# Kernel optimization log

Hardware: AMD Instinct MI355X
Metric: run time of the kernel (lower is better)

## Reference

```python
import jax, jax.numpy as jnp
import numpy as np

L, C = 32768, 512
EPS = 1e-5

def _layernorm(x, w, b):
    mu = jnp.mean(x, axis=-1, keepdims=True)
    var = jnp.mean(jnp.square(x - mu), axis=-1, keepdims=True)
    return (x - mu) * jax.lax.rsqrt(var + EPS) * w + b

def _scan(u, decay):
    # inclusive first-order linear scan: b_t = decay * b_{t-1} + u_t
    a = jnp.broadcast_to(decay, u.shape)
    def combine(l, r):
        return (l[0] * r[0], r[1] + r[0] * l[1])
    _, b = jax.lax.associative_scan(combine, (a, u), axis=0)
    return b

def setup_inputs() -> dict:
    key = jax.random.key(0)
    ks = jax.random.split(key, 8)
    s = 0.02
    return {
        "x": jax.random.normal(ks[0], (L, C), dtype=jnp.float32),
        "ln1_w": jnp.ones((C,), jnp.float32),
        "ln1_b": jnp.zeros((C,), jnp.float32),
        "W_in": jax.random.normal(ks[1], (C, C), jnp.float32) * s,
        "b_in": jnp.zeros((C,), jnp.float32),
        "W_gate": jax.random.normal(ks[2], (C, C), jnp.float32) * s,
        "b_gate": jnp.zeros((C,), jnp.float32),
        "W_out": jax.random.normal(ks[3], (C, C), jnp.float32) * s,
        "b_out": jnp.zeros((C,), jnp.float32),
        "decay_logit": jnp.zeros((C,), jnp.float32),  # torch init: zeros -> sigmoid = 0.5
        "ln2_w": jnp.ones((C,), jnp.float32),
        "ln2_b": jnp.zeros((C,), jnp.float32),
        "W_ff1": jax.random.normal(ks[4], (C, 2 * C), jnp.float32) * s,
        "b_ff1": jnp.zeros((2 * C,), jnp.float32),
        "W_ff2": jax.random.normal(ks[5], (2 * C, C), jnp.float32) * s,
        "b_ff2": jnp.zeros((C,), jnp.float32),
    }

def reference(x, ln1_w, ln1_b, W_in, b_in, W_gate, b_gate, W_out, b_out,
              decay_logit, ln2_w, ln2_b, W_ff1, b_ff1, W_ff2, b_ff2):
    hidden = _layernorm(x, ln1_w, ln1_b)
    u = hidden @ W_in + b_in
    gate = jax.nn.sigmoid(hidden @ W_gate + b_gate)
    decay = jax.nn.sigmoid(decay_logit)
    fwd = _scan(u, decay) * gate
    bwd = jnp.flip(_scan(jnp.flip(u, axis=0), decay), axis=0) * gate
    state_out = 0.5 * (fwd + bwd)
    x = x + state_out @ W_out + b_out
    h = _layernorm(x, ln2_w, ln2_b)
    x = x + jax.nn.silu(h @ W_ff1 + b_ff1) @ W_ff2 + b_ff2
    return x
```

## Files before the change

### kernel.cpp

```cpp
#include <hip/hip_runtime.h>
#include <stdint.h>


#define L_SEQ 32768
#define CDIM 512
#define LN_EPS 1e-5f
#define CHUNK 64
#define NCHUNK (L_SEQ / CHUNK)

typedef __attribute__((ext_vector_type(8))) short short8;
typedef __attribute__((ext_vector_type(4))) float floatx4;

__device__ inline unsigned short f2bf(float f) {
  union { float f; unsigned int u; } v; v.f = f;
  unsigned int r = v.u + 0x7fffu + ((v.u >> 16) & 1u);
  return (unsigned short)(r >> 16);
}
__device__ inline float bf2f(unsigned short h) {
  union { float f; unsigned int u; } v; v.u = ((unsigned int)h) << 16;
  return v.f;
}
__device__ inline float sigmoidf_(float x) { return 1.0f / (1.0f + __expf(-x)); }

__device__ inline void async16(const void* g, void* l) {
  __builtin_amdgcn_global_load_lds(
      (const __attribute__((address_space(1))) unsigned int*)g,
      (__attribute__((address_space(3))) unsigned int*)l, 16, 0, 0);
}

__global__ __launch_bounds__(256) void ln_kernel(const float* __restrict__ x,
    const float* __restrict__ w, const float* __restrict__ b,
    unsigned short* __restrict__ out) {
  int row = blockIdx.x * 4 + (threadIdx.x >> 6);
  int lane = threadIdx.x & 63;
  const float4* xr = (const float4*)(x + (size_t)row * CDIM);
  float4 v0 = xr[lane * 2];
  float4 v1 = xr[lane * 2 + 1];
  float s = v0.x + v0.y + v0.z + v0.w + v1.x + v1.y + v1.z + v1.w;
  float s2 = v0.x * v0.x + v0.y * v0.y + v0.z * v0.z + v0.w * v0.w +
             v1.x * v1.x + v1.y * v1.y + v1.z * v1.z + v1.w * v1.w;
  for (int m = 32; m > 0; m >>= 1) {
    s += __shfl_xor(s, m, 64);
    s2 += __shfl_xor(s2, m, 64);
  }
  float mean = s * (1.0f / CDIM);
  float var = s2 * (1.0f / CDIM) - mean * mean;
  float rs = rsqrtf(var + LN_EPS);
  const float4* wr = (const float4*)w;
  const float4* br = (const float4*)b;
  float4 w0 = wr[lane * 2], w1 = wr[lane * 2 + 1];
  float4 b0 = br[lane * 2], b1 = br[lane * 2 + 1];
  unsigned int p0 = (unsigned int)f2bf((v0.x - mean) * rs * w0.x + b0.x) |
                    ((unsigned int)f2bf((v0.y - mean) * rs * w0.y + b0.y) << 16);
  unsigned int p1 = (unsigned int)f2bf((v0.z - mean) * rs * w0.z + b0.z) |
                    ((unsigned int)f2bf((v0.w - mean) * rs * w0.w + b0.w) << 16);
  unsigned int p2 = (unsigned int)f2bf((v1.x - mean) * rs * w1.x + b1.x) |
                    ((unsigned int)f2bf((v1.y - mean) * rs * w1.y + b1.y) << 16);
  unsigned int p3 = (unsigned int)f2bf((v1.z - mean) * rs * w1.z + b1.z) |
                    ((unsigned int)f2bf((v1.w - mean) * rs * w1.w + b1.w) << 16);
  uint4 pk; pk.x = p0; pk.y = p1; pk.z = p2; pk.w = p3;
  *((uint4*)(out + (size_t)row * CDIM + lane * 8)) = pk;
}

__global__ __launch_bounds__(256) void transpose_w(const float* __restrict__ W,
    unsigned short* __restrict__ Wt, int K, int N) {
  __shared__ float tile[32][33];
  int n0 = blockIdx.x * 32, k0 = blockIdx.y * 32;
  int tx = threadIdx.x & 31, ty = threadIdx.x >> 5;
  for (int r = 0; r < 32; r += 8)
    tile[ty + r][tx] = W[(size_t)(k0 + ty + r) * N + n0 + tx];
  __syncthreads();
  for (int r = 0; r < 32; r += 8)
    Wt[(size_t)(n0 + ty + r) * K + k0 + tx] = f2bf(tile[tx][ty + r]);
}

__global__ void decay_prep(const float* __restrict__ logit,
    float* __restrict__ decay, float* __restrict__ decayT) {
  int c = threadIdx.x;
  float d = sigmoidf_(logit[c]);
  decay[c] = d;
  float p = d;
  for (int i = 0; i < 6; i++) p *= p;
  decayT[c] = p;
}

template <int EPI>
__global__ __launch_bounds__(256, 3) void gemm_bt(
    const unsigned short* __restrict__ A, const unsigned short* __restrict__ Bt,
    const float* __restrict__ biasA, const float* __restrict__ biasB,
    const float* __restrict__ res, float* __restrict__ outF,
    unsigned short* __restrict__ outU, unsigned short* __restrict__ outG,
    int M, int N, int K) {
  __shared__ unsigned short As[2][128 * 32];
  __shared__ unsigned short Bs[2][128 * 32];

  int nbx = gridDim.x, nby = gridDim.y;
  int bid = blockIdx.x + blockIdx.y * nbx;
  int per = (nbx * nby) >> 3;
  int w = (bid & 7) * per + (bid >> 3);
  int ni = w % nby;
  int mi = w / nby;
  int bm = mi << 7, bn = ni << 7;

  int tid = threadIdx.x, wave = tid >> 6, lane = tid & 63;
  int wm = (wave >> 1) * 64, wn = (wave & 1) * 64;

  int srow = wave * 16 + (lane >> 2);
  int scol = (lane & 3) * 8;
  const unsigned short* aP0 = A + (size_t)(bm + srow) * K + scol;
  const unsigned short* aP1 = A + (size_t)(bm + 64 + srow) * K + scol;
  const unsigned short* bP0 = Bt + (size_t)(bn + srow) * K + scol;
  const unsigned short* bP1 = Bt + (size_t)(bn + 64 + srow) * K + scol;

  floatx4 acc[4][4];
#pragma unroll
  for (int i = 0; i < 4; i++)
#pragma unroll
    for (int j = 0; j < 4; j++) acc[i][j] = (floatx4){0.f, 0.f, 0.f, 0.f};

  int quad = lane >> 4, r16 = lane & 15;

  async16(aP0, &As[0][wave * 512]);
  async16(aP1, &As[0][2048 + wave * 512]);
  async16(bP0, &Bs[0][wave * 512]);
  async16(bP1, &Bs[0][2048 + wave * 512]);

  for (int k0 = 0; k0 < K; k0 += 32) {
    int cur = (k0 >> 5) & 1, nxt = cur ^ 1;
    __syncthreads();
    if (k0 + 32 < K) {
      async16(aP0 + k0 + 32, &As[nxt][wave * 512]);
      async16(aP1 + k0 + 32, &As[nxt][2048 + wave * 512]);
      async16(bP0 + k0 + 32, &Bs[nxt][wave * 512]);
      async16(bP1 + k0 + 32, &Bs[nxt][2048 + wave * 512]);
    }
    short8 af[4], bfm[4];
#pragma unroll
    for (int i = 0; i < 4; i++)
      af[i] = *(const short8*)(&As[cur][(wm + i * 16 + r16) * 32 + quad * 8]);
#pragma unroll
    for (int j = 0; j < 4; j++)
      bfm[j] = *(const short8*)(&Bs[cur][(wn + j * 16 + r16) * 32 + quad * 8]);
#pragma unroll
    for (int i = 0; i < 4; i++)
#pragma unroll
      for (int j = 0; j < 4; j++)
        acc[i][j] = __builtin_amdgcn_mfma_f32_16x16x32_bf16(af[i], bfm[j], acc[i][j], 0, 0, 0);
  }

#pragma unroll
  for (int j = 0; j < 4; j++) {
    int n = bn + wn + j * 16 + r16;
#pragma unroll
    for (int i = 0; i < 4; i++) {
      int mb = bm + wm + i * 16 + quad * 4;
#pragma unroll
      for (int r = 0; r < 4; r++) {
        int m = mb + r;
        float v = acc[i][j][r];
        if (EPI == 0) {
          if (n < 512) {
            outU[(size_t)m * 512 + n] = f2bf(v + biasA[n]);
          } else {
            outG[(size_t)m * 512 + (n - 512)] = f2bf(sigmoidf_(v + biasB[n - 512]));
          }
        } else if (EPI == 1) {
          size_t idx = (size_t)m * N + n;
          outF[idx] = res[idx] + v + biasA[n];
        } else {
          float t = v + biasA[n];
          outG[(size_t)m * N + n] = f2bf(t * sigmoidf_(t));
        }
      }
    }
  }
}

__global__ __launch_bounds__(512) void scan_phase1(const unsigned short* __restrict__ u,
    const float* __restrict__ decay, float* __restrict__ fa, float* __restrict__ ba) {
  int c = threadIdx.x, k = blockIdx.x;
  float d = decay[c];
  const unsigned short* up = u + (size_t)k * CHUNK * CDIM + c;
  float f = 0.f, bs = 0.f, p = 1.f;
#pragma unroll 8
  for (int t = 0; t < CHUNK; t++) {
    float v = bf2f(up[(size_t)t * CDIM]);
    f = d * f + v;
    bs += p * v;
    p *= d;
  }
  fa[(size_t)k * CDIM + c] = f;
  ba[(size_t)k * CDIM + c] = bs;
}

__global__ __launch_bounds__(256) void scan_phase2(const float* __restrict__ fa,
    const float* __restrict__ ba, const float* __restrict__ decayT,
    float* __restrict__ fc, float* __restrict__ bc) {
  int c = blockIdx.x * 256 + threadIdx.x;
  float dT = decayT[c];
  float run = 0.f;
#pragma unroll 8
  for (int k = 0; k < NCHUNK; k++) {
    fc[(size_t)k * CDIM + c] = run;
    run = dT * run + fa[(size_t)k * CDIM + c];
  }
  run = 0.f;
#pragma unroll 8
  for (int k = NCHUNK - 1; k >= 0; k--) {
    bc[(size_t)k * CDIM + c] = run;
    run = dT * run + ba[(size_t)k * CDIM + c];
  }
}

__global__ __launch_bounds__(512) void scan_phase3(const unsigned short* __restrict__ u,
    const unsigned short* __restrict__ gate, const float* __restrict__ decay,
    const float* __restrict__ fc, const float* __restrict__ bc,
    unsigned short* __restrict__ state) {
  int c = threadIdx.x, k = blockIdx.x;
  float d = decay[c];
  size_t base = (size_t)k * CHUNK * CDIM + c;
  float fwd[CHUNK];
  float run = fc[(size_t)k * CDIM + c];
#pragma unroll
  for (int t = 0; t < CHUNK; t++) {
    run = d * run + bf2f(u[base + (size_t)t * CDIM]);
    fwd[t] = run;
  }
  float runb = bc[(size_t)k * CDIM + c];
#pragma unroll
  for (int t = CHUNK - 1; t >= 0; t--) {
    runb = d * runb + bf2f(u[base + (size_t)t * CDIM]);
    float g = bf2f(gate[base + (size_t)t * CDIM]);
    state[base + (size_t)t * CDIM] = f2bf(0.5f * (fwd[t] + runb) * g);
  }
}

extern "C" void kernel_launch(void* const* d_in, const int* in_sizes, int n_in,
                              void* d_out, int out_size, void* d_ws, size_t ws_size,
                              hipStream_t stream) {
  const float* x = (const float*)d_in[0];
  const float* ln1_w = (const float*)d_in[1];
  const float* ln1_b = (const float*)d_in[2];
  const float* W_in = (const float*)d_in[3];
  const float* b_in = (const float*)d_in[4];
  const float* W_gate = (const float*)d_in[5];
  const float* b_gate = (const float*)d_in[6];
  const float* W_out = (const float*)d_in[7];
  const float* b_out = (const float*)d_in[8];
  const float* decay_logit = (const float*)d_in[9];
  const float* ln2_w = (const float*)d_in[10];
  const float* ln2_b = (const float*)d_in[11];
  const float* W_ff1 = (const float*)d_in[12];
  const float* b_ff1 = (const float*)d_in[13];
  const float* W_ff2 = (const float*)d_in[14];
  const float* b_ff2 = (const float*)d_in[15];

  char* ws = (char*)d_ws;
  size_t off = 0;
  auto alloc = [&](size_t bytes) -> void* {
    void* p = ws + off;
    off += (bytes + 255) & ~(size_t)255;
    return p;
  };
  unsigned short* Wt_ig  = (unsigned short*)alloc((size_t)1024 * 512 * 2);
  unsigned short* Wt_out = (unsigned short*)alloc((size_t)512 * 512 * 2);
  unsigned short* Wt_ff1 = (unsigned short*)alloc((size_t)1024 * 512 * 2);
  unsigned short* Wt_ff2 = (unsigned short*)alloc((size_t)512 * 1024 * 2);
  float* fa = (float*)alloc((size_t)NCHUNK * CDIM * 4);
  float* ba = (float*)alloc((size_t)NCHUNK * CDIM * 4);
  float* fc = (float*)alloc((size_t)NCHUNK * CDIM * 4);
  float* bc = (float*)alloc((size_t)NCHUNK * CDIM * 4);
  float* decay  = (float*)alloc(CDIM * 4);
  float* decayT = (float*)alloc(CDIM * 4);
  const size_t LC2 = (size_t)L_SEQ * CDIM * 2;
  unsigned short* R1 = (unsigned short*)alloc(LC2);
  unsigned short* R2 = (unsigned short*)alloc(LC2);
  unsigned short* R3 = (unsigned short*)alloc(LC2);
  unsigned short* hidden = R1;
  unsigned short* state  = R1;
  unsigned short* hbuf   = R1;
  unsigned short* u_buf  = R2;
  unsigned short* gate   = R3;
  unsigned short* ffb    = R2;
  float* x2 = (float*)d_out;

  transpose_w<<<dim3(16, 16), 256, 0, stream>>>(W_in, Wt_ig, 512, 512);
  transpose_w<<<dim3(16, 16), 256, 0, stream>>>(W_gate, Wt_ig + 512 * 512, 512, 512);
  transpose_w<<<dim3(16, 16), 256, 0, stream>>>(W_out, Wt_out, 512, 512);
  transpose_w<<<dim3(32, 16), 256, 0, stream>>>(W_ff1, Wt_ff1, 512, 1024);
  transpose_w<<<dim3(16, 32), 256, 0, stream>>>(W_ff2, Wt_ff2, 1024, 512);
  decay_prep<<<1, 512, 0, stream>>>(decay_logit, decay, decayT);

  ln_kernel<<<L_SEQ / 4, 256, 0, stream>>>(x, ln1_w, ln1_b, hidden);

  gemm_bt<0><<<dim3(L_SEQ / 128, 1024 / 128), 256, 0, stream>>>(
      hidden, Wt_ig, b_in, b_gate, nullptr, nullptr, u_buf, gate, L_SEQ, 1024, 512);

  scan_phase1<<<NCHUNK, 512, 0, stream>>>(u_buf, decay, fa, ba);
  scan_phase2<<<2, 256, 0, stream>>>(fa, ba, decayT, fc, bc);
  scan_phase3<<<NCHUNK, 512, 0, stream>>>(u_buf, gate, decay, fc, bc, state);

  gemm_bt<1><<<dim3(L_SEQ / 128, 512 / 128), 256, 0, stream>>>(
      state, Wt_out, b_out, nullptr, x, x2, nullptr, nullptr, L_SEQ, 512, 512);

  ln_kernel<<<L_SEQ / 4, 256, 0, stream>>>(x2, ln2_w, ln2_b, hbuf);

  gemm_bt<2><<<dim3(L_SEQ / 128, 1024 / 128), 256, 0, stream>>>(
      hbuf, Wt_ff1, b_ff1, nullptr, nullptr, nullptr, nullptr, ffb, L_SEQ, 1024, 512);

  gemm_bt<1><<<dim3(L_SEQ / 128, 512 / 128), 256, 0, stream>>>(
      ffb, Wt_ff2, b_ff2, nullptr, x2, x2, nullptr, nullptr, L_SEQ, 512, 1024);
}
```

Measured before the change: 499.2 us.

## Swizzle GEMM LDS tiles and stage bf16 epilogue through shared memory

The GEMM now uses a single raw shared buffer with an XOR-swizzled column layout for the A/B tiles, so fragment reads hit fewer LDS bank conflicts. For the bf16-output epilogues (in-proj/gate and FF1 SiLU), results are first written to a padded shared tile and then copied out with 16-byte vector stores per row, replacing scattered 2-byte global stores. Occupancy hint raised from 3 to 4 blocks per CU. The larger shared footprint (about 34 KB) and extra barriers may limit the occupancy gain.

```diff
diff --git a/kernel.cpp b/kernel.cpp
--- a/kernel.cpp
+++ b/kernel.cpp
@@ -85,14 +85,15 @@
 }
 
 template <int EPI>
-__global__ __launch_bounds__(256, 3) void gemm_bt(
+__global__ __launch_bounds__(256, 4) void gemm_bt(
     const unsigned short* __restrict__ A, const unsigned short* __restrict__ Bt,
     const float* __restrict__ biasA, const float* __restrict__ biasB,
     const float* __restrict__ res, float* __restrict__ outF,
     unsigned short* __restrict__ outU, unsigned short* __restrict__ outG,
     int M, int N, int K) {
-  __shared__ unsigned short As[2][128 * 32];
-  __shared__ unsigned short Bs[2][128 * 32];
+  __shared__ char smemRaw[34048];
+  unsigned short* As = (unsigned short*)smemRaw;
+  unsigned short* Bs = (unsigned short*)(smemRaw + 16384);
 
   int nbx = gridDim.x, nby = gridDim.y;
   int bid = blockIdx.x + blockIdx.y * nbx;
@@ -106,7 +107,8 @@
   int wm = (wave >> 1) * 64, wn = (wave & 1) * 64;
 
   int srow = wave * 16 + (lane >> 2);
-  int scol = (lane & 3) * 8;
+  int chunkSel = (lane & 3) ^ ((lane >> 3) & 3);
+  int scol = chunkSel * 8;
   const unsigned short* aP0 = A + (size_t)(bm + srow) * K + scol;
   const unsigned short* aP1 = A + (size_t)(bm + 64 + srow) * K + scol;
   const unsigned short* bP0 = Bt + (size_t)(bn + srow) * K + scol;
@@ -119,28 +121,29 @@
     for (int j = 0; j < 4; j++) acc[i][j] = (floatx4){0.f, 0.f, 0.f, 0.f};
 
   int quad = lane >> 4, r16 = lane & 15;
-
-  async16(aP0, &As[0][wave * 512]);
-  async16(aP1, &As[0][2048 + wave * 512]);
-  async16(bP0, &Bs[0][wave * 512]);
-  async16(bP1, &Bs[0][2048 + wave * 512]);
+  int cSwz = ((quad ^ (r16 >> 1)) & 3) * 8;
+
+  async16(aP0, &As[wave * 512]);
+  async16(aP1, &As[2048 + wave * 512]);
+  async16(bP0, &Bs[wave * 512]);
+  async16(bP1, &Bs[2048 + wave * 512]);
 
   for (int k0 = 0; k0 < K; k0 += 32) {
-    int cur = (k0 >> 5) & 1, nxt = cur ^ 1;
+    int cur = ((k0 >> 5) & 1) * 4096, nxt = cur ^ 4096;
     __syncthreads();
     if (k0 + 32 < K) {
-      async16(aP0 + k0 + 32, &As[nxt][wave * 512]);
-      async16(aP1 + k0 + 32, &As[nxt][2048 + wave * 512]);
-      async16(bP0 + k0 + 32, &Bs[nxt][wave * 512]);
-      async16(bP1 + k0 + 32, &Bs[nxt][2048 + wave * 512]);
+      async16(aP0 + k0 + 32, &As[nxt + wave * 512]);
+      async16(aP1 + k0 + 32, &As[nxt + 2048 + wave * 512]);
+      async16(bP0 + k0 + 32, &Bs[nxt + wave * 512]);
+      async16(bP1 + k0 + 32, &Bs[nxt + 2048 + wave * 512]);
     }
     short8 af[4], bfm[4];
 #pragma unroll
     for (int i = 0; i < 4; i++)
-      af[i] = *(const short8*)(&As[cur][(wm + i * 16 + r16) * 32 + quad * 8]);
+      af[i] = *(const short8*)(&As[cur + (wm + i * 16 + r16) * 32 + cSwz]);
 #pragma unroll
     for (int j = 0; j < 4; j++)
-      bfm[j] = *(const short8*)(&Bs[cur][(wn + j * 16 + r16) * 32 + quad * 8]);
+      bfm[j] = *(const short8*)(&Bs[cur + (wn + j * 16 + r16) * 32 + cSwz]);
 #pragma unroll
     for (int i = 0; i < 4; i++)
 #pragma unroll
@@ -148,31 +151,56 @@
         acc[i][j] = __builtin_amdgcn_mfma_f32_16x16x32_bf16(af[i], bfm[j], acc[i][j], 0, 0, 0);
   }
 
-#pragma unroll
-  for (int j = 0; j < 4; j++) {
-    int n = bn + wn + j * 16 + r16;
-#pragma unroll
-    for (int i = 0; i < 4; i++) {
-      int mb = bm + wm + i * 16 + quad * 4;
-#pragma unroll
-      for (int r = 0; r < 4; r++) {
-        int m = mb + r;
-        float v = acc[i][j][r];
-        if (EPI == 0) {
-          if (n < 512) {
-            outU[(size_t)m * 512 + n] = f2bf(v + biasA[n]);
-          } else {
-            outG[(size_t)m * 512 + (n - 512)] = f2bf(sigmoidf_(v + biasB[n - 512]));
-          }
-        } else if (EPI == 1) {
-          size_t idx = (size_t)m * N + n;
-          outF[idx] = res[idx] + v + biasA[n];
-        } else {
-          float t = v + biasA[n];
-          outG[(size_t)m * N + n] = f2bf(t * sigmoidf_(t));
+  if (EPI == 1) {
+#pragma unroll
+    for (int j = 0; j < 4; j++) {
+      int n = bn + wn + j * 16 + r16;
+#pragma unroll
+      for (int i = 0; i < 4; i++) {
+        int mb = bm + wm + i * 16 + quad * 4;
+#pragma unroll
+        for (int r = 0; r < 4; r++) {
+          size_t idx = (size_t)(mb + r) * N + n;
+          outF[idx] = res[idx] + acc[i][j][r] + biasA[n];
         }
       }
     }
+  } else {
+    unsigned short* sm = (unsigned short*)smemRaw;
+    __syncthreads();
+#pragma unroll
+    for (int j = 0; j < 4; j++) {
+      int n = bn + wn + j * 16 + r16;
+      int ln = wn + j * 16 + r16;
+#pragma unroll
+      for (int i = 0; i < 4; i++) {
+        int lmb = wm + i * 16 + quad * 4;
+#pragma unroll
+        for (int r = 0; r < 4; r++) {
+          float v = acc[i][j][r];
+          float t;
+          if (EPI == 0) {
+            t = (n < 512) ? (v + biasA[n]) : sigmoidf_(v + biasB[n - 512]);
+          } else {
+            float z = v + biasA[n];
+            t = z * sigmoidf_(z);
+          }
+          sm[(lmb + r) * 132 + ln] = f2bf(t);
+        }
+      }
+    }
+    __syncthreads();
+    int row = tid >> 1, half = tid & 1;
+    const unsigned short* src = sm + row * 132 + half * 64;
+    unsigned short* gptr;
+    if (EPI == 0) {
+      gptr = ((bn < 512) ? outU : (outG - 512)) + (size_t)(bm + row) * 512 + bn + half * 64;
+    } else {
+      gptr = outG + (size_t)(bm + row) * N + bn + half * 64;
+    }
+#pragma unroll
+    for (int s = 0; s < 8; s++)
+      *(short8*)(gptr + s * 8) = *(const short8*)(src + s * 8);
   }
 }
 
```

After: 496.4 us. Within noise of the previous version (-0.6%).
